# Optimization experiments

Measured on AMD Instinct MI355X. Metric: run time of the kernel, lower is better.

## Reference

```python
import jax, jax.numpy as jnp
import numpy as np

LN2 = float(np.log(2.0))
CUTOFF_L = 0.5


def _ssp(x):
    # shifted softplus: log(0.5*exp(x) + 0.5)
    return jax.nn.softplus(x) - LN2


def _pair_idx(n):
    # ordered pairs arranged [n, n-1]: for each i, all j != i
    idx = np.arange(n)
    j = np.stack([np.concatenate([idx[:k], idx[k + 1:]]) for k in range(n)])  # [n, n-1]
    i = np.broadcast_to(idx[:, None], j.shape)
    return jnp.asarray(i), jnp.asarray(j)


def _mlp3(x, w1, b1, w2, b2, w3, b3):
    h = _ssp(x @ w1 + b1)
    h = _ssp(h @ w2 + b2)
    return h @ w3 + b3


def _backflow_cutoff(r, L=CUTOFF_L):
    r = r / L
    return jnp.where(r < L, r ** 2 * (6.0 - 8.0 * r + 3.0 * r ** 2), jnp.ones((), r.dtype))


def setup_inputs() -> dict:
    key = jax.random.key(0)
    ks = jax.random.split(key, 12)
    B, N, D, K = 512, 32, 256, 8
    dims_e = [D, 40, 6, 1]
    dims_n = [D, 81, 25, 8]

    def lin(k, fi, fo):
        return jax.random.normal(k, (fi, fo), jnp.float32) / np.sqrt(fi)

    inp = {
        'rs': jax.random.normal(ks[0], (B, N, 3), jnp.float32),
        'xs': jax.random.normal(ks[1], (B, N, D), jnp.float32),
        'coords': jax.random.normal(ks[2], (K, 3), jnp.float32) * 2.0,
        'ew1': lin(ks[3], dims_e[0], dims_e[1]), 'eb1': jnp.zeros((dims_e[1],), jnp.float32),
        'ew2': lin(ks[4], dims_e[1], dims_e[2]), 'eb2': jnp.zeros((dims_e[2],), jnp.float32),
        'ew3': lin(ks[5], dims_e[2], dims_e[3]), 'eb3': jnp.zeros((dims_e[3],), jnp.float32),
        'nw1': lin(ks[6], dims_n[0], dims_n[1]), 'nb1': jnp.zeros((dims_n[1],), jnp.float32),
        'nw2': lin(ks[7], dims_n[1], dims_n[2]), 'nb2': jnp.zeros((dims_n[2],), jnp.float32),
        'nw3': lin(ks[8], dims_n[2], dims_n[3]), 'nb3': jnp.zeros((dims_n[3],), jnp.float32),
    }
    return inp


def reference(rs, xs, coords, ew1, eb1, ew2, eb2, ew3, eb3,
              nw1, nb1, nw2, nb2, nw3, nb3):
    n_elec = rs.shape[-2]
    i, j = _pair_idx(n_elec)  # [n, n-1] static index arrays

    # electron-electron backflow
    diffs_elec = rs[..., i, :] - rs[..., j, :]                    # [B, n, n-1, 3]
    pair_feat = xs[..., i, :] * xs[..., j, :]                     # [B, n, n-1, D]
    w_pair = _mlp3(pair_feat, ew1, eb1, ew2, eb2, ew3, eb3)       # [B, n, n-1, 1]
    bf_elec = (w_pair * diffs_elec).sum(axis=-2)                  # [B, n, 3]

    # electron-nucleus backflow
    diffs_nuc = rs[..., :, None, :] - coords                      # [B, n, K, 3]
    w_nuc = _mlp3(xs, nw1, nb1, nw2, nb2, nw3, nb3)               # [B, n, K]
    bf_nuc = (w_nuc[..., None] * diffs_nuc).sum(axis=-2)          # [B, n, 3]

    dist_nuc = jnp.linalg.norm(diffs_nuc, axis=-1)                # [B, n, K]
    cutoff = _backflow_cutoff(dist_nuc).prod(axis=-1)             # [B, n]

    return rs + 1e-4 * cutoff[..., None] * (bf_elec + bf_nuc)
```

## Files before the change

kernel.cpp:

```cpp
#include <hip/hip_runtime.h>
#include <stdint.h>

static constexpr int B_ = 512, N_ = 32, D_ = 256, K_ = 8;
static constexpr int E1 = 40, E2 = 6;
static constexpr int N1 = 81, N2 = 25, N3 = 8;
static constexpr int XBP = 264;
static constexpr int HEP = 96;
static constexpr int EWT = 264;
static constexpr int TKP = 48;
static constexpr int NWP = 104;
static constexpr int TILE16 = 16 * TKP;
static constexpr float LN2f  = 0.69314718055994530942f;
static constexpr float L2Ef  = 1.44269504088896340736f;

typedef float    f32x4 __attribute__((ext_vector_type(4)));
typedef _Float16 f16x8 __attribute__((ext_vector_type(8)));
typedef _Float16 f16x4 __attribute__((ext_vector_type(4)));

#if __has_builtin(__builtin_amdgcn_mfma_f32_16x16x16_f16)
#define MFMA16(A, B, C) __builtin_amdgcn_mfma_f32_16x16x16_f16((A), (B), (C), 0, 0, 0)
#else
#define MFMA16(A, B, C) __builtin_amdgcn_mfma_f32_16x16x16f16((A), (B), (C), 0, 0, 0)
#endif

__device__ __forceinline__ float ssp2(float t) {
    float e = __builtin_amdgcn_exp2f(t);
    return __builtin_amdgcn_logf(fmaf(e, 0.5f, 0.5f));
}

__global__ __launch_bounds__(512) void k_fused(
    const float* __restrict__ rs, const float* __restrict__ xs,
    const float* __restrict__ coords,
    const float* __restrict__ ew1, const float* __restrict__ eb1,
    const float* __restrict__ ew2, const float* __restrict__ eb2,
    const float* __restrict__ ew3, const float* __restrict__ eb3,
    const float* __restrict__ nw1, const float* __restrict__ nb1,
    const float* __restrict__ nw2, const float* __restrict__ nb2,
    const float* __restrict__ nw3, const float* __restrict__ nb3,
    float* __restrict__ out)
{
    __shared__ alignas(16) _Float16 xs_h[N_ * XBP];
    __shared__ alignas(16) _Float16 wbuf[E1 * EWT];
    __shared__ alignas(16) char uni[18688];
    __shared__ float nw3_s[N2 * N3];
    __shared__ float rs_s[N_ * 3];
    __shared__ float nb2_s[N2];
    __shared__ float nb3_s[N3];
    __shared__ float co_s[K_ * 3];
    __shared__ float bfn_s[N_ * 3];
    __shared__ float cut_s[N_];
    __shared__ float bfe_s[N_ * 3];
    __shared__ alignas(16) float eb1_s[48];
    __shared__ alignas(16) float b2_s[16];

    _Float16* h1e  = (_Float16*)(uni + 9216);
    float*    h2e  = (float*)(uni + 15360);
    _Float16* nw2T = (_Float16*)uni;

    const int b = blockIdx.x, t = threadIdx.x;
    const int wv = t >> 6, l = t & 63, quad = l >> 4, c = l & 15;

    f16x4 b2fT[3];
    #pragma unroll
    for (int Nt = 0; Nt < 3; ++Nt) {
        f16x4 p;
        #pragma unroll
        for (int r = 0; r < 4; ++r) {
            int n = Nt * 16 + quad * 4 + r;
            p[r] = (_Float16)((n < E1 && c < E2) ? ew2[n * E2 + c] : 0.f);
        }
        b2fT[Nt] = p;
    }
    float w3q[4];
    #pragma unroll
    for (int r = 0; r < 4; ++r) {
        int m = quad * 4 + r;
        w3q[r] = (m < E2) ? ew3[m] * LN2f : 0.f;
    }
    const float eb3v = eb3[0];

    {
        const float4* src = (const float4*)(xs + (size_t)b * N_ * D_);
        #pragma unroll
        for (int u = 0; u < 4; ++u) {
            int q = t + 512 * u;
            float4 v = src[q];
            int row = q >> 6, col4 = q & 63;
            union { _Float16 h[4]; uint64_t u64; } pk;
            pk.h[0] = (_Float16)v.x; pk.h[1] = (_Float16)v.y;
            pk.h[2] = (_Float16)v.z; pk.h[3] = (_Float16)v.w;
            *(uint64_t*)&xs_h[row * XBP + col4 * 4] = pk.u64;
        }
    }
    {
        const float4* src = (const float4*)ew1;
        #pragma unroll
        for (int u = 0; u < 5; ++u) {
            int q = t + 512 * u;
            float4 v = src[q];
            int k = q / 10, n0 = (q - 10 * k) * 4;
            wbuf[(n0 + 0) * EWT + k] = (_Float16)(v.x * L2Ef);
            wbuf[(n0 + 1) * EWT + k] = (_Float16)(v.y * L2Ef);
            wbuf[(n0 + 2) * EWT + k] = (_Float16)(v.z * L2Ef);
            wbuf[(n0 + 3) * EWT + k] = (_Float16)(v.w * L2Ef);
        }
    }
    if (t < 128) {
        int m = t >> 2, q4 = t & 3;
        *(uint64_t*)(uni + 9216 + m * (HEP * 2) + 160 + q4 * 8) = 0ull;
    }
    if (t < N_ * 3) rs_s[t] = rs[b * N_ * 3 + t];
    if (t < N2 * N3) nw3_s[t] = nw3[t] * LN2f;
    if (t < N2) nb2_s[t] = nb2[t] * L2Ef;
    if (t < N3) nb3_s[t] = nb3[t];
    if (t < K_ * 3) co_s[t] = coords[t];
    if (t < 48) eb1_s[t] = (t < E1) ? eb1[t] * L2Ef : 0.f;
    if (t < 16) b2_s[t] = (t < E2) ? eb2[t] * L2Ef : 0.f;
    __syncthreads();

    if (wv < 6) {
        _Float16* tile = (_Float16*)uni + wv * TILE16;
        const int ln = l & 15, lq = l >> 4;
        const int gn = wv * 16 + ln;
        const bool gok = (gn < N1);
        const int n_col = wv * 16 + c;
        const float nb1v = (n_col < N1) ? nb1[n_col] * L2Ef : 0.f;

        float pf[8];
        #pragma unroll
        for (int u = 0; u < 8; ++u)
            pf[u] = gok ? nw1[(lq + 4 * u) * N1 + gn] : 0.f;

        f32x4 acc[2];
        acc[0] = (f32x4){0.f, 0.f, 0.f, 0.f};
        acc[1] = (f32x4){0.f, 0.f, 0.f, 0.f};

        #pragma unroll 1
        for (int Kt = 0; Kt < 8; ++Kt) {
            #pragma unroll
            for (int u = 0; u < 8; ++u)
                tile[ln * TKP + lq + 4 * u] = (_Float16)(pf[u] * L2Ef);
            if (Kt < 7) {
                const float* wk = nw1 + (Kt + 1) * 32 * N1 + gn;
                #pragma unroll
                for (int u = 0; u < 8; ++u)
                    pf[u] = gok ? wk[(lq + 4 * u) * N1] : 0.f;
            }
            f16x8 Bf = *(const f16x8*)&tile[c * TKP + quad * 8];
            #pragma unroll
            for (int Mt = 0; Mt < 2; ++Mt) {
                f16x8 A = *(const f16x8*)&xs_h[(Mt * 16 + c) * XBP + Kt * 32 + quad * 8];
                acc[Mt] = __builtin_amdgcn_mfma_f32_16x16x32_f16(A, Bf, acc[Mt], 0, 0, 0);
            }
        }
        if (n_col < N1) {
            #pragma unroll
            for (int Mt = 0; Mt < 2; ++Mt)
                #pragma unroll
                for (int r2 = 0; r2 < 4; ++r2) {
                    int m = Mt * 16 + quad * 4 + r2;
                    h1e[m * HEP + n_col] = (_Float16)ssp2(acc[Mt][r2] + nb1v);
                }
        }
    }
    __syncthreads();

    f16x8 b1f[3][8];
    #pragma unroll
    for (int Nt = 0; Nt < 3; ++Nt) {
        int n = Nt * 16 + c;
        bool ok = (n < E1);
        int row = ok ? n : 0;
        #pragma unroll
        for (int Kt = 0; Kt < 8; ++Kt) {
            f16x8 v = *(const f16x8*)&wbuf[row * EWT + Kt * 32 + quad * 8];
            if (!ok) v = (f16x8)(_Float16)0.f;
            b1f[Nt][Kt] = v;
        }
    }
    #pragma unroll
    for (int u = 0; u < 6; ++u) {
        int idx = t + 512 * u;
        int n = idx / 96, kk = idx - 96 * n;
        float v = (kk < N1 && n < N2) ? nw2[kk * N2 + n] : 0.f;
        nw2T[n * NWP + kk] = (_Float16)v;
    }
    __syncthreads();

    if (wv < 4) {
        const int Mt = wv & 1, Nt = wv >> 1;
        f32x4 acc2 = {0.f, 0.f, 0.f, 0.f};
        #pragma unroll
        for (int Kt2 = 0; Kt2 < 3; ++Kt2) {
            f16x8 A  = *(const f16x8*)&h1e[(Mt * 16 + c) * HEP + Kt2 * 32 + quad * 8];
            f16x8 Bf = *(const f16x8*)&nw2T[(Nt * 16 + c) * NWP + Kt2 * 32 + quad * 8];
            acc2 = __builtin_amdgcn_mfma_f32_16x16x32_f16(A, Bf, acc2, 0, 0, 0);
        }
        int n = Nt * 16 + c;
        if (n < N2) {
            #pragma unroll
            for (int r2 = 0; r2 < 4; ++r2) {
                int m = Mt * 16 + quad * 4 + r2;
                h2e[m * 26 + n] = ssp2(acc2[r2] + nb2_s[n]);
            }
        }
    }
    __syncthreads();

    if (t < 256) {
        const int r = t >> 3, s = t & 7;
        float w = nb3_s[s];
        const int rb = r * 26;
        #pragma unroll
        for (int kk = 0; kk < N2; ++kk)
            w = fmaf(h2e[rb + kk], nw3_s[kk * N3 + s], w);

        float dx = rs_s[r * 3 + 0] - co_s[s * 3 + 0];
        float dy = rs_s[r * 3 + 1] - co_s[s * 3 + 1];
        float dz = rs_s[r * 3 + 2] - co_s[s * 3 + 2];
        float cx = w * dx, cy = w * dy, cz = w * dz;
        #pragma unroll
        for (int m2 = 1; m2 < 8; m2 <<= 1) {
            cx += __shfl_xor(cx, m2);
            cy += __shfl_xor(cy, m2);
            cz += __shfl_xor(cz, m2);
        }
        float rr  = sqrtf(dx * dx + dy * dy + dz * dz);
        float xsc = 2.f * rr;
        float cf  = (xsc < 0.5f) ? xsc * xsc * (6.f - 8.f * xsc + 3.f * xsc * xsc) : 1.f;
        #pragma unroll
        for (int m2 = 1; m2 < 8; m2 <<= 1) cf *= __shfl_xor(cf, m2);
        if (s == 0) {
            bfn_s[r * 3 + 0] = cx;
            bfn_s[r * 3 + 1] = cy;
            bfn_s[r * 3 + 2] = cz;
            cut_s[r] = cf;
        }
    }

    #pragma unroll 1
    for (int q8 = 0; q8 < 4; ++q8) {
        const int i = wv + 8 * q8;
        f32x4 acc[2][3];
        #pragma unroll
        for (int Nt = 0; Nt < 3; ++Nt) {
            f32x4 bias = *(const f32x4*)&eb1_s[Nt * 16 + quad * 4];
            acc[0][Nt] = bias;
            acc[1][Nt] = bias;
        }

        #pragma unroll
        for (int Kt = 0; Kt < 8; ++Kt) {
            const int koff = Kt * 32 + quad * 8;
            f16x8 iv  = *(const f16x8*)&xs_h[i * XBP + koff];
            f16x8 jv0 = *(const f16x8*)&xs_h[c * XBP + koff];
            f16x8 jv1 = *(const f16x8*)&xs_h[(16 + c) * XBP + koff];
            f16x8 P0 = iv * jv0;
            f16x8 P1 = iv * jv1;
            #pragma unroll
            for (int Nt = 0; Nt < 3; ++Nt) {
                acc[0][Nt] = __builtin_amdgcn_mfma_f32_16x16x32_f16(b1f[Nt][Kt], P0, acc[0][Nt], 0, 0, 0);
                acc[1][Nt] = __builtin_amdgcn_mfma_f32_16x16x32_f16(b1f[Nt][Kt], P1, acc[1][Nt], 0, 0, 0);
            }
        }

        const float rix = rs_s[i * 3 + 0], riy = rs_s[i * 3 + 1], riz = rs_s[i * 3 + 2];
        float cxi = 0.f, cyi = 0.f, czi = 0.f;
        const f32x4 b2i = *(const f32x4*)&b2_s[quad * 4];
        #pragma unroll
        for (int h = 0; h < 2; ++h) {
            f32x4 acc2 = b2i;
            #pragma unroll
            for (int Nt = 0; Nt < 3; ++Nt) {
                f16x4 bh;
                #pragma unroll
                for (int r2 = 0; r2 < 4; ++r2)
                    bh[r2] = (_Float16)ssp2(acc[h][Nt][r2]);
                acc2 = MFMA16(b2fT[Nt], bh, acc2);
            }
            float ws = 0.f;
            #pragma unroll
            for (int r2 = 0; r2 < 4; ++r2)
                ws = fmaf(w3q[r2], ssp2(acc2[r2]), ws);
            ws += __shfl_xor(ws, 16);
            ws += __shfl_xor(ws, 32);
            float wj = ws + eb3v;
            int j = c + 16 * h;
            cxi = fmaf(wj, rix - rs_s[j * 3 + 0], cxi);
            cyi = fmaf(wj, riy - rs_s[j * 3 + 1], cyi);
            czi = fmaf(wj, riz - rs_s[j * 3 + 2], czi);
        }
        #pragma unroll
        for (int m2 = 1; m2 < 16; m2 <<= 1) {
            cxi += __shfl_xor(cxi, m2);
            cyi += __shfl_xor(cyi, m2);
            czi += __shfl_xor(czi, m2);
        }
        if (l == 0) {
            bfe_s[i * 3 + 0] = cxi;
            bfe_s[i * 3 + 1] = cyi;
            bfe_s[i * 3 + 2] = czi;
        }
    }
    __syncthreads();

    if (t < N_ * 3) {
        int i = t / 3;
        out[(size_t)b * (N_ * 3) + t] =
            rs_s[t] + 1e-4f * cut_s[i] * (bfe_s[t] + bfn_s[t]);
    }
}

extern "C" void kernel_launch(void* const* d_in, const int* in_sizes, int n_in,
                              void* d_out, int out_size, void* d_ws, size_t ws_size,
                              hipStream_t stream)
{
    const float* rs     = (const float*)d_in[0];
    const float* xs     = (const float*)d_in[1];
    const float* coords = (const float*)d_in[2];
    const float* ew1    = (const float*)d_in[3];
    const float* eb1    = (const float*)d_in[4];
    const float* ew2    = (const float*)d_in[5];
    const float* eb2    = (const float*)d_in[6];
    const float* ew3    = (const float*)d_in[7];
    const float* eb3    = (const float*)d_in[8];
    const float* nw1    = (const float*)d_in[9];
    const float* nb1    = (const float*)d_in[10];
    const float* nw2    = (const float*)d_in[11];
    const float* nb2    = (const float*)d_in[12];
    const float* nw3    = (const float*)d_in[13];
    const float* nb3    = (const float*)d_in[14];

    k_fused<<<B_, 512, 0, stream>>>(rs, xs, coords, ew1, eb1, ew2, eb2, ew3, eb3,
                                    nw1, nb1, nw2, nb2, nw3, nb3, (float*)d_out);
}
```

Measured before the change: 130.3 us.

## Split each batch across two blocks, pretranspose weights in a prep kernel, swizzle LDS

```diff
diff --git a/kernel.cpp b/kernel.cpp
--- a/kernel.cpp
+++ b/kernel.cpp
@@ -1,22 +1,19 @@
 #include <hip/hip_runtime.h>
 #include <stdint.h>
+
 
 static constexpr int B_ = 512, N_ = 32, D_ = 256, K_ = 8;
 static constexpr int E1 = 40, E2 = 6;
 static constexpr int N1 = 81, N2 = 25, N3 = 8;
-static constexpr int XBP = 264;
 static constexpr int HEP = 96;
-static constexpr int EWT = 264;
-static constexpr int TKP = 48;
-static constexpr int NWP = 104;
-static constexpr int TILE16 = 16 * TKP;
-static constexpr float LN2f  = 0.69314718055994530942f;
-static constexpr float L2Ef  = 1.44269504088896340736f;
+static constexpr float LN2f = 0.69314718055994530942f;
+static constexpr float L2Ef = 1.44269504088896340736f;
 
 typedef float    f32x4 __attribute__((ext_vector_type(4)));
 typedef _Float16 f16x8 __attribute__((ext_vector_type(8)));
 typedef _Float16 f16x4 __attribute__((ext_vector_type(4)));
 
+#define MFMA32(A, B, C) __builtin_amdgcn_mfma_f32_16x16x32_f16((A), (B), (C), 0, 0, 0)
 #if __has_builtin(__builtin_amdgcn_mfma_f32_16x16x16_f16)
 #define MFMA16(A, B, C) __builtin_amdgcn_mfma_f32_16x16x16_f16((A), (B), (C), 0, 0, 0)
 #else
@@ -28,37 +25,114 @@
     return __builtin_amdgcn_logf(fmaf(e, 0.5f, 0.5f));
 }
 
-__global__ __launch_bounds__(512) void k_fused(
+__device__ __forceinline__ void lds_dma16(void* lds, const void* g) {
+    __builtin_amdgcn_global_load_lds(
+        (const __attribute__((address_space(1))) unsigned int*)(uintptr_t)g,
+        (__attribute__((address_space(3))) unsigned int*)(uintptr_t)lds,
+        16, 0, 0);
+}
+
+__global__ __launch_bounds__(256) void k_prep(
+    const float* __restrict__ ew1, const float* __restrict__ nw1,
+    const float* __restrict__ nw2, _Float16* __restrict__ wsp)
+{
+    const int g = blockIdx.x * 256 + threadIdx.x;
+    _Float16* ew1T = wsp;
+    _Float16* nw1T = wsp + 48 * 256;
+    _Float16* nw2T = wsp + 48 * 256 + 96 * 256;
+
+    if (g < 1536) {
+        const int n = g >> 5, kb = g & 31;
+        f16x8 v;
+        #pragma unroll
+        for (int d = 0; d < 8; ++d) {
+            const int k = kb * 8 + d;
+            v[d] = (_Float16)((n < E1) ? ew1[k * E1 + n] * L2Ef : 0.f);
+        }
+        *(f16x8*)&ew1T[n * 256 + ((kb ^ (n & 7)) << 3)] = v;
+    } else if (g < 4608) {
+        const int q = g - 1536;
+        const int n = q >> 5, kb = q & 31;
+        f16x8 v;
+        #pragma unroll
+        for (int d = 0; d < 8; ++d) {
+            const int k = kb * 8 + d;
+            v[d] = (_Float16)((n < N1) ? nw1[k * N1 + n] * L2Ef : 0.f);
+        }
+        *(f16x8*)&nw1T[n * 256 + kb * 8] = v;
+    } else if (g < 4992) {
+        const int q = g - 4608;
+        const int n = q / 12, kb = q - n * 12;
+        f16x8 v;
+        #pragma unroll
+        for (int d = 0; d < 8; ++d) {
+            const int kk = kb * 8 + d;
+            v[d] = (_Float16)((n < N2 && kk < N1) ? nw2[kk * N2 + n] : 0.f);
+        }
+        *(f16x8*)&nw2T[n * 96 + kb * 8] = v;
+    }
+}
+
+__global__ __launch_bounds__(512, 6) void k_fused(
     const float* __restrict__ rs, const float* __restrict__ xs,
     const float* __restrict__ coords,
-    const float* __restrict__ ew1, const float* __restrict__ eb1,
-    const float* __restrict__ ew2, const float* __restrict__ eb2,
-    const float* __restrict__ ew3, const float* __restrict__ eb3,
-    const float* __restrict__ nw1, const float* __restrict__ nb1,
-    const float* __restrict__ nw2, const float* __restrict__ nb2,
-    const float* __restrict__ nw3, const float* __restrict__ nb3,
+    const float* __restrict__ eb1, const float* __restrict__ ew2,
+    const float* __restrict__ eb2, const float* __restrict__ ew3,
+    const float* __restrict__ eb3, const float* __restrict__ nb1,
+    const float* __restrict__ nb2, const float* __restrict__ nb3,
+    const float* __restrict__ nw3, const _Float16* __restrict__ wsp,
     float* __restrict__ out)
 {
-    __shared__ alignas(16) _Float16 xs_h[N_ * XBP];
-    __shared__ alignas(16) _Float16 wbuf[E1 * EWT];
-    __shared__ alignas(16) char uni[18688];
-    __shared__ float nw3_s[N2 * N3];
-    __shared__ float rs_s[N_ * 3];
-    __shared__ float nb2_s[N2];
-    __shared__ float nb3_s[N3];
-    __shared__ float co_s[K_ * 3];
-    __shared__ float bfn_s[N_ * 3];
-    __shared__ float cut_s[N_];
-    __shared__ float bfe_s[N_ * 3];
-    __shared__ alignas(16) float eb1_s[48];
-    __shared__ alignas(16) float b2_s[16];
-
-    _Float16* h1e  = (_Float16*)(uni + 9216);
-    float*    h2e  = (float*)(uni + 15360);
-    _Float16* nw2T = (_Float16*)uni;
-
-    const int b = blockIdx.x, t = threadIdx.x;
+    __shared__ alignas(16) _Float16 xs_h[N_ * 256];
+    __shared__ alignas(16) _Float16 ew1T_s[48 * 256];
+    __shared__ alignas(16) _Float16 h1e[16 * HEP];
+    __shared__ alignas(16) float    h2e[16 * 26];
+    __shared__ alignas(16) float    eb1_s[48];
+    __shared__ alignas(16) float    b2_s[16];
+    __shared__ float rs_s[96], nw3_s[200], nb2_s[32], nb3_s[8], co_s[24];
+    __shared__ float bfn_s[48], cut_s[16], bfe_s[48];
+
+    const int bid = blockIdx.x;
+    const int b = bid >> 1, rbase = (bid & 1) << 4;
+    const int t = threadIdx.x;
     const int wv = t >> 6, l = t & 63, quad = l >> 4, c = l & 15;
+
+    const _Float16* ew1T_g = wsp;
+    const _Float16* nw1T_g = wsp + 48 * 256;
+    const _Float16* nw2T_g = wsp + 48 * 256 + 96 * 256;
+
+    {
+        const char* g = (const char*)ew1T_g;
+        char* d = (char*)ew1T_s;
+        const int wb = wv * 1024;
+        #pragma unroll
+        for (int r = 0; r < 3; ++r)
+            lds_dma16(d + r * 8192 + wb, g + r * 8192 + wb + (l << 4));
+    }
+    {
+        const float4* src = (const float4*)(xs + (size_t)b * N_ * D_);
+        #pragma unroll
+        for (int u = 0; u < 2; ++u) {
+            const int idx = t + 512 * u;
+            const int row = idx >> 5, kb = idx & 31;
+            float4 v0 = src[idx << 1];
+            float4 v1 = src[(idx << 1) + 1];
+            union { _Float16 h[8]; uint4 q; } pk;
+            pk.h[0] = (_Float16)v0.x; pk.h[1] = (_Float16)v0.y;
+            pk.h[2] = (_Float16)v0.z; pk.h[3] = (_Float16)v0.w;
+            pk.h[4] = (_Float16)v1.x; pk.h[5] = (_Float16)v1.y;
+            pk.h[6] = (_Float16)v1.z; pk.h[7] = (_Float16)v1.w;
+            *(uint4*)&xs_h[row * 256 + ((kb ^ (row & 7)) << 3)] = pk.q;
+        }
+    }
+    if (t < 96)  rs_s[t] = rs[b * 96 + t];
+    if (t < 200) nw3_s[t] = nw3[t] * LN2f;
+    if (t < N2)  nb2_s[t] = nb2[t] * L2Ef;
+    if (t < N3)  nb3_s[t] = nb3[t];
+    if (t < 24)  co_s[t] = coords[t];
+    if (t < 48)  eb1_s[t] = (t < E1) ? eb1[t] * L2Ef : 0.f;
+    if (t < 16)  b2_s[t] = (t < E2) ? eb2[t] * L2Ef : 0.f;
+    if (t < 384) ((uint64_t*)h1e)[t] = 0ull;
 
     f16x4 b2fT[3];
     #pragma unroll
@@ -66,7 +140,7 @@
         f16x4 p;
         #pragma unroll
         for (int r = 0; r < 4; ++r) {
-            int n = Nt * 16 + quad * 4 + r;
+            const int n = Nt * 16 + quad * 4 + r;
             p[r] = (_Float16)((n < E1 && c < E2) ? ew2[n * E2 + c] : 0.f);
         }
         b2fT[Nt] = p;
@@ -74,150 +148,130 @@
     float w3q[4];
     #pragma unroll
     for (int r = 0; r < 4; ++r) {
-        int m = quad * 4 + r;
+        const int m = quad * 4 + r;
         w3q[r] = (m < E2) ? ew3[m] * LN2f : 0.f;
     }
     const float eb3v = eb3[0];
 
-    {
-        const float4* src = (const float4*)(xs + (size_t)b * N_ * D_);
-        #pragma unroll
-        for (int u = 0; u < 4; ++u) {
-            int q = t + 512 * u;
-            float4 v = src[q];
-            int row = q >> 6, col4 = q & 63;
-            union { _Float16 h[4]; uint64_t u64; } pk;
-            pk.h[0] = (_Float16)v.x; pk.h[1] = (_Float16)v.y;
-            pk.h[2] = (_Float16)v.z; pk.h[3] = (_Float16)v.w;
-            *(uint64_t*)&xs_h[row * XBP + col4 * 4] = pk.u64;
-        }
-    }
-    {
-        const float4* src = (const float4*)ew1;
-        #pragma unroll
-        for (int u = 0; u < 5; ++u) {
-            int q = t + 512 * u;
-            float4 v = src[q];
-            int k = q / 10, n0 = (q - 10 * k) * 4;
-            wbuf[(n0 + 0) * EWT + k] = (_Float16)(v.x * L2Ef);
-            wbuf[(n0 + 1) * EWT + k] = (_Float16)(v.y * L2Ef);
-            wbuf[(n0 + 2) * EWT + k] = (_Float16)(v.z * L2Ef);
-            wbuf[(n0 + 3) * EWT + k] = (_Float16)(v.w * L2Ef);
-        }
-    }
-    if (t < 128) {
-        int m = t >> 2, q4 = t & 3;
-        *(uint64_t*)(uni + 9216 + m * (HEP * 2) + 160 + q4 * 8) = 0ull;
-    }
-    if (t < N_ * 3) rs_s[t] = rs[b * N_ * 3 + t];
-    if (t < N2 * N3) nw3_s[t] = nw3[t] * LN2f;
-    if (t < N2) nb2_s[t] = nb2[t] * L2Ef;
-    if (t < N3) nb3_s[t] = nb3[t];
-    if (t < K_ * 3) co_s[t] = coords[t];
-    if (t < 48) eb1_s[t] = (t < E1) ? eb1[t] * L2Ef : 0.f;
-    if (t < 16) b2_s[t] = (t < E2) ? eb2[t] * L2Ef : 0.f;
     __syncthreads();
 
+    auto ee_round = [&](int lr) {
+        const int i = rbase + lr;
+        f32x4 acc[2][3];
+        #pragma unroll
+        for (int Nt = 0; Nt < 3; ++Nt) {
+            f32x4 bias = *(const f32x4*)&eb1_s[Nt * 16 + quad * 4];
+            acc[0][Nt] = bias;
+            acc[1][Nt] = bias;
+        }
+        #pragma unroll
+        for (int Kt = 0; Kt < 8; ++Kt) {
+            const int kb = Kt * 4 + quad;
+            const int sj = (kb ^ (c & 7)) << 3;
+            f16x8 iv  = *(const f16x8*)&xs_h[i * 256 + ((kb ^ (i & 7)) << 3)];
+            f16x8 jv0 = *(const f16x8*)&xs_h[c * 256 + sj];
+            f16x8 jv1 = *(const f16x8*)&xs_h[(16 + c) * 256 + sj];
+            f16x8 P0 = iv * jv0;
+            f16x8 P1 = iv * jv1;
+            #pragma unroll
+            for (int Nt = 0; Nt < 3; ++Nt) {
+                f16x8 b1 = *(const f16x8*)&ew1T_s[(Nt * 16 + c) * 256 + sj];
+                acc[0][Nt] = MFMA32(b1, P0, acc[0][Nt]);
+                acc[1][Nt] = MFMA32(b1, P1, acc[1][Nt]);
+            }
+        }
+        const float rix = rs_s[i * 3 + 0], riy = rs_s[i * 3 + 1], riz = rs_s[i * 3 + 2];
+        float cxi = 0.f, cyi = 0.f, czi = 0.f;
+        const f32x4 b2i = *(const f32x4*)&b2_s[quad * 4];
+        #pragma unroll
+        for (int h = 0; h < 2; ++h) {
+            f32x4 acc2 = b2i;
+            #pragma unroll
+            for (int Nt = 0; Nt < 3; ++Nt) {
+                f16x4 bh_;
+                #pragma unroll
+                for (int r2 = 0; r2 < 4; ++r2)
+                    bh_[r2] = (_Float16)ssp2(acc[h][Nt][r2]);
+                acc2 = MFMA16(b2fT[Nt], bh_, acc2);
+            }
+            float wsum = 0.f;
+            #pragma unroll
+            for (int r2 = 0; r2 < 4; ++r2)
+                wsum = fmaf(w3q[r2], ssp2(acc2[r2]), wsum);
+            wsum += __shfl_xor(wsum, 16);
+            wsum += __shfl_xor(wsum, 32);
+            const float wj = wsum + eb3v;
+            const int j = c + 16 * h;
+            cxi = fmaf(wj, rix - rs_s[j * 3 + 0], cxi);
+            cyi = fmaf(wj, riy - rs_s[j * 3 + 1], cyi);
+            czi = fmaf(wj, riz - rs_s[j * 3 + 2], czi);
+        }
+        #pragma unroll
+        for (int m2 = 1; m2 < 16; m2 <<= 1) {
+            cxi += __shfl_xor(cxi, m2);
+            cyi += __shfl_xor(cyi, m2);
+            czi += __shfl_xor(czi, m2);
+        }
+        if (l == 0) {
+            bfe_s[lr * 3 + 0] = cxi;
+            bfe_s[lr * 3 + 1] = cyi;
+            bfe_s[lr * 3 + 2] = czi;
+        }
+    };
+
     if (wv < 6) {
-        _Float16* tile = (_Float16*)uni + wv * TILE16;
-        const int ln = l & 15, lq = l >> 4;
-        const int gn = wv * 16 + ln;
-        const bool gok = (gn < N1);
         const int n_col = wv * 16 + c;
         const float nb1v = (n_col < N1) ? nb1[n_col] * L2Ef : 0.f;
-
-        float pf[8];
-        #pragma unroll
-        for (int u = 0; u < 8; ++u)
-            pf[u] = gok ? nw1[(lq + 4 * u) * N1 + gn] : 0.f;
-
-        f32x4 acc[2];
-        acc[0] = (f32x4){0.f, 0.f, 0.f, 0.f};
-        acc[1] = (f32x4){0.f, 0.f, 0.f, 0.f};
-
-        #pragma unroll 1
+        const _Float16* bg = nw1T_g + n_col * 256 + quad * 8;
+        f32x4 acc1 = (f32x4){0.f, 0.f, 0.f, 0.f};
+        f16x8 Bp = *(const f16x8*)bg;
+        #pragma unroll
         for (int Kt = 0; Kt < 8; ++Kt) {
-            #pragma unroll
-            for (int u = 0; u < 8; ++u)
-                tile[ln * TKP + lq + 4 * u] = (_Float16)(pf[u] * L2Ef);
-            if (Kt < 7) {
-                const float* wk = nw1 + (Kt + 1) * 32 * N1 + gn;
-                #pragma unroll
-                for (int u = 0; u < 8; ++u)
-                    pf[u] = gok ? wk[(lq + 4 * u) * N1] : 0.f;
-            }
-            f16x8 Bf = *(const f16x8*)&tile[c * TKP + quad * 8];
-            #pragma unroll
-            for (int Mt = 0; Mt < 2; ++Mt) {
-                f16x8 A = *(const f16x8*)&xs_h[(Mt * 16 + c) * XBP + Kt * 32 + quad * 8];
-                acc[Mt] = __builtin_amdgcn_mfma_f32_16x16x32_f16(A, Bf, acc[Mt], 0, 0, 0);
-            }
+            f16x8 Bf = Bp;
+            if (Kt < 7) Bp = *(const f16x8*)(bg + (Kt + 1) * 32);
+            f16x8 A = *(const f16x8*)&xs_h[(rbase + c) * 256 +
+                                           (((Kt * 4 + quad) ^ (c & 7)) << 3)];
+            acc1 = MFMA32(A, Bf, acc1);
         }
         if (n_col < N1) {
             #pragma unroll
-            for (int Mt = 0; Mt < 2; ++Mt)
-                #pragma unroll
-                for (int r2 = 0; r2 < 4; ++r2) {
-                    int m = Mt * 16 + quad * 4 + r2;
-                    h1e[m * HEP + n_col] = (_Float16)ssp2(acc[Mt][r2] + nb1v);
-                }
-        }
-    }
+            for (int r2 = 0; r2 < 4; ++r2)
+                h1e[(quad * 4 + r2) * HEP + n_col] = (_Float16)ssp2(acc1[r2] + nb1v);
+        }
+    }
+    ee_round(wv);
     __syncthreads();
 
-    f16x8 b1f[3][8];
-    #pragma unroll
-    for (int Nt = 0; Nt < 3; ++Nt) {
-        int n = Nt * 16 + c;
-        bool ok = (n < E1);
-        int row = ok ? n : 0;
-        #pragma unroll
-        for (int Kt = 0; Kt < 8; ++Kt) {
-            f16x8 v = *(const f16x8*)&wbuf[row * EWT + Kt * 32 + quad * 8];
-            if (!ok) v = (f16x8)(_Float16)0.f;
-            b1f[Nt][Kt] = v;
-        }
-    }
-    #pragma unroll
-    for (int u = 0; u < 6; ++u) {
-        int idx = t + 512 * u;
-        int n = idx / 96, kk = idx - 96 * n;
-        float v = (kk < N1 && n < N2) ? nw2[kk * N2 + n] : 0.f;
-        nw2T[n * NWP + kk] = (_Float16)v;
-    }
+    if (wv < 2) {
+        const int n = wv * 16 + c;
+        const _Float16* bg2 = nw2T_g + n * 96 + quad * 8;
+        f32x4 acc2 = (f32x4){0.f, 0.f, 0.f, 0.f};
+        #pragma unroll
+        for (int Kt2 = 0; Kt2 < 3; ++Kt2) {
+            f16x8 A  = *(const f16x8*)&h1e[c * HEP + Kt2 * 32 + quad * 8];
+            f16x8 Bf = *(const f16x8*)(bg2 + Kt2 * 32);
+            acc2 = MFMA32(A, Bf, acc2);
+        }
+        if (n < N2) {
+            #pragma unroll
+            for (int r2 = 0; r2 < 4; ++r2)
+                h2e[(quad * 4 + r2) * 26 + n] = ssp2(acc2[r2] + nb2_s[n]);
+        }
+    }
+    ee_round(wv + 8);
     __syncthreads();
 
-    if (wv < 4) {
-        const int Mt = wv & 1, Nt = wv >> 1;
-        f32x4 acc2 = {0.f, 0.f, 0.f, 0.f};
-        #pragma unroll
-        for (int Kt2 = 0; Kt2 < 3; ++Kt2) {
-            f16x8 A  = *(const f16x8*)&h1e[(Mt * 16 + c) * HEP + Kt2 * 32 + quad * 8];
-            f16x8 Bf = *(const f16x8*)&nw2T[(Nt * 16 + c) * NWP + Kt2 * 32 + quad * 8];
-            acc2 = __builtin_amdgcn_mfma_f32_16x16x32_f16(A, Bf, acc2, 0, 0, 0);
-        }
-        int n = Nt * 16 + c;
-        if (n < N2) {
-            #pragma unroll
-            for (int r2 = 0; r2 < 4; ++r2) {
-                int m = Mt * 16 + quad * 4 + r2;
-                h2e[m * 26 + n] = ssp2(acc2[r2] + nb2_s[n]);
-            }
-        }
-    }
-    __syncthreads();
-
-    if (t < 256) {
+    if (t < 128) {
         const int r = t >> 3, s = t & 7;
+        const int gi = rbase + r;
         float w = nb3_s[s];
-        const int rb = r * 26;
+        const int rb26 = r * 26;
         #pragma unroll
         for (int kk = 0; kk < N2; ++kk)
-            w = fmaf(h2e[rb + kk], nw3_s[kk * N3 + s], w);
-
-        float dx = rs_s[r * 3 + 0] - co_s[s * 3 + 0];
-        float dy = rs_s[r * 3 + 1] - co_s[s * 3 + 1];
-        float dz = rs_s[r * 3 + 2] - co_s[s * 3 + 2];
+            w = fmaf(h2e[rb26 + kk], nw3_s[kk * N3 + s], w);
+        const float dx = rs_s[gi * 3 + 0] - co_s[s * 3 + 0];
+        const float dy = rs_s[gi * 3 + 1] - co_s[s * 3 + 1];
+        const float dz = rs_s[gi * 3 + 2] - co_s[s * 3 + 2];
         float cx = w * dx, cy = w * dy, cz = w * dz;
         #pragma unroll
         for (int m2 = 1; m2 < 8; m2 <<= 1) {
@@ -225,9 +279,9 @@
             cy += __shfl_xor(cy, m2);
             cz += __shfl_xor(cz, m2);
         }
-        float rr  = sqrtf(dx * dx + dy * dy + dz * dz);
-        float xsc = 2.f * rr;
-        float cf  = (xsc < 0.5f) ? xsc * xsc * (6.f - 8.f * xsc + 3.f * xsc * xsc) : 1.f;
+        const float rr  = sqrtf(dx * dx + dy * dy + dz * dz);
+        const float xsc = 2.f * rr;
+        float cf = (xsc < 0.5f) ? xsc * xsc * (6.f - 8.f * xsc + 3.f * xsc * xsc) : 1.f;
         #pragma unroll
         for (int m2 = 1; m2 < 8; m2 <<= 1) cf *= __shfl_xor(cf, m2);
         if (s == 0) {
@@ -237,77 +291,12 @@
             cut_s[r] = cf;
         }
     }
-
-    #pragma unroll 1
-    for (int q8 = 0; q8 < 4; ++q8) {
-        const int i = wv + 8 * q8;
-        f32x4 acc[2][3];
-        #pragma unroll
-        for (int Nt = 0; Nt < 3; ++Nt) {
-            f32x4 bias = *(const f32x4*)&eb1_s[Nt * 16 + quad * 4];
-            acc[0][Nt] = bias;
-            acc[1][Nt] = bias;
-        }
-
-        #pragma unroll
-        for (int Kt = 0; Kt < 8; ++Kt) {
-            const int koff = Kt * 32 + quad * 8;
-            f16x8 iv  = *(const f16x8*)&xs_h[i * XBP + koff];
-            f16x8 jv0 = *(const f16x8*)&xs_h[c * XBP + koff];
-            f16x8 jv1 = *(const f16x8*)&xs_h[(16 + c) * XBP + koff];
-            f16x8 P0 = iv * jv0;
-            f16x8 P1 = iv * jv1;
-            #pragma unroll
-            for (int Nt = 0; Nt < 3; ++Nt) {
-                acc[0][Nt] = __builtin_amdgcn_mfma_f32_16x16x32_f16(b1f[Nt][Kt], P0, acc[0][Nt], 0, 0, 0);
-                acc[1][Nt] = __builtin_amdgcn_mfma_f32_16x16x32_f16(b1f[Nt][Kt], P1, acc[1][Nt], 0, 0, 0);
-            }
-        }
-
-        const float rix = rs_s[i * 3 + 0], riy = rs_s[i * 3 + 1], riz = rs_s[i * 3 + 2];
-        float cxi = 0.f, cyi = 0.f, czi = 0.f;
-        const f32x4 b2i = *(const f32x4*)&b2_s[quad * 4];
-        #pragma unroll
-        for (int h = 0; h < 2; ++h) {
-            f32x4 acc2 = b2i;
-            #pragma unroll
-            for (int Nt = 0; Nt < 3; ++Nt) {
-                f16x4 bh;
-                #pragma unroll
-                for (int r2 = 0; r2 < 4; ++r2)
-                    bh[r2] = (_Float16)ssp2(acc[h][Nt][r2]);
-                acc2 = MFMA16(b2fT[Nt], bh, acc2);
-            }
-            float ws = 0.f;
-            #pragma unroll
-            for (int r2 = 0; r2 < 4; ++r2)
-                ws = fmaf(w3q[r2], ssp2(acc2[r2]), ws);
-            ws += __shfl_xor(ws, 16);
-            ws += __shfl_xor(ws, 32);
-            float wj = ws + eb3v;
-            int j = c + 16 * h;
-            cxi = fmaf(wj, rix - rs_s[j * 3 + 0], cxi);
-            cyi = fmaf(wj, riy - rs_s[j * 3 + 1], cyi);
-            czi = fmaf(wj, riz - rs_s[j * 3 + 2], czi);
-        }
-        #pragma unroll
-        for (int m2 = 1; m2 < 16; m2 <<= 1) {
-            cxi += __shfl_xor(cxi, m2);
-            cyi += __shfl_xor(cyi, m2);
-            czi += __shfl_xor(czi, m2);
-        }
-        if (l == 0) {
-            bfe_s[i * 3 + 0] = cxi;
-            bfe_s[i * 3 + 1] = cyi;
-            bfe_s[i * 3 + 2] = czi;
-        }
-    }
     __syncthreads();
 
-    if (t < N_ * 3) {
-        int i = t / 3;
-        out[(size_t)b * (N_ * 3) + t] =
-            rs_s[t] + 1e-4f * cut_s[i] * (bfe_s[t] + bfn_s[t]);
+    if (t < 48) {
+        const int r = t / 3;
+        out[(size_t)b * (N_ * 3) + rbase * 3 + t] =
+            rs_s[rbase * 3 + t] + 1e-4f * cut_s[r] * (bfe_s[t] + bfn_s[t]);
     }
 }
 
@@ -331,6 +320,9 @@
     const float* nw3    = (const float*)d_in[13];
     const float* nb3    = (const float*)d_in[14];
 
-    k_fused<<<B_, 512, 0, stream>>>(rs, xs, coords, ew1, eb1, ew2, eb2, ew3, eb3,
-                                    nw1, nb1, nw2, nb2, nw3, nb3, (float*)d_out);
-}
+    _Float16* wsp = (_Float16*)d_ws;
+
+    k_prep<<<20, 256, 0, stream>>>(ew1, nw1, nw2, wsp);
+    k_fused<<<B_ * 2, 512, 0, stream>>>(rs, xs, coords, eb1, ew2, eb2, ew3, eb3,
+                                        nb1, nb2, nb3, nw3, wsp, (float*)d_out);
+}
```

New measurement: 131.1 us. Within noise of the previous version (+0.6%).
